# Performance work log

Measured on AMD Instinct MI355X. Metric: run time of the kernel, lower is better.

The kernel has to match this reference:

```python
import jax, jax.numpy as jnp
import numpy as np
from jax.ops import segment_sum

N_NODES = 50000


def graph_conv(src, dst, x, W, b, n_nodes):
    # DGL GraphConv with norm='both' (allow_zero_in_degree=True):
    # h = D_in^{-1/2} * A^T (D_out^{-1/2} * x) W + b, degrees clamped to >=1
    ones = jnp.ones(src.shape[0], dtype=x.dtype)
    deg_out = jnp.clip(segment_sum(ones, src, num_segments=n_nodes), 1.0)
    deg_in = jnp.clip(segment_sum(ones, dst, num_segments=n_nodes), 1.0)
    h = x * jax.lax.rsqrt(deg_out)[:, None]
    h = h @ W                      # apply weight before aggregation (mult_W first)
    m = segment_sum(h[src], dst, num_segments=n_nodes)  # sparse neighbor sum
    return m * jax.lax.rsqrt(deg_in)[:, None] + b


def setup_inputs() -> dict:
    key = jax.random.key(0)
    ks = jax.random.split(key, 10)
    n, e = N_NODES, 1600000
    d_in, h1, h2, h3 = 128, 128, 128, 64
    in_feat = jax.random.normal(ks[0], (n, d_in), dtype=jnp.float32)
    src = jax.random.randint(ks[1], (e,), 0, n, dtype=jnp.int32)
    dst = jax.random.randint(ks[2], (e,), 0, n, dtype=jnp.int32)
    s = lambda fi, fo: (1.0 / np.sqrt(fi)).astype(np.float32)
    W1 = jax.random.normal(ks[3], (d_in, h1), dtype=jnp.float32) * s(d_in, h1)
    b1 = jnp.zeros((h1,), dtype=jnp.float32)
    W2 = jax.random.normal(ks[4], (h1, h2), dtype=jnp.float32) * s(h1, h2)
    b2 = jnp.zeros((h2,), dtype=jnp.float32)
    Wf = jax.random.normal(ks[5], (h2, h3), dtype=jnp.float32) * s(h2, h3)
    bf = jnp.zeros((h3,), dtype=jnp.float32)
    return {"in_feat": in_feat, "src": src, "dst": dst,
            "W1": W1, "b1": b1, "W2": W2, "b2": b2, "Wf": Wf, "bf": bf}


def reference(in_feat, src, dst, W1, b1, W2, b2, Wf, bf):
    n = in_feat.shape[0]
    h = graph_conv(src, dst, in_feat, W1, b1, n)
    h = jax.nn.relu(h)
    # dropout(p=0.2) is identity in eval mode
    h = graph_conv(src, dst, h, W2, b2, n)
    return h @ Wf + bf
```

## Files before the change

### kernel.cpp

```cpp
#include <hip/hip_runtime.h>
#include <hip/hip_fp16.h>

#define FD 128
#define OD 64
#define KC 8
#define RN 256
#define CHUNKS 256
#define NRMAX 1024

typedef _Float16 f16x8 __attribute__((ext_vector_type(8)));
typedef float    f32x4 __attribute__((ext_vector_type(4)));


__global__ void zero_kernel(int* __restrict__ a, int n) {
    int i = blockIdx.x * 256 + threadIdx.x;
    if (i < n) a[i] = 0;
}

__global__ void rout_kernel(const int* __restrict__ cnt, float* __restrict__ r_out,
                            int N, int NW) {
    int v = blockIdx.x * 256 + threadIdx.x;
    if (v >= N) return;
    int word = v >> 1, sh = (v & 1) * 16;
    int s = 0;
    #pragma unroll
    for (int k = 0; k < KC; k++) s += (cnt[k * NW + word] >> sh) & 0xFFFF;
    r_out[v] = rsqrtf((float)max(s, 1));
}

__global__ void prescale_kernel(const float* __restrict__ X, const float* __restrict__ r_out,
                                __half* __restrict__ Xs, int n4) {
    int i = blockIdx.x * 256 + threadIdx.x;
    if (i >= n4) return;
    int v = i >> 5;
    float r = r_out[v];
    float4 t = ((const float4*)X)[i];
    __half2 h0 = __floats2half2_rn(t.x * r, t.y * r);
    __half2 h1 = __floats2half2_rn(t.z * r, t.w * r);
    ((__half2*)Xs)[2 * i]     = h0;
    ((__half2*)Xs)[2 * i + 1] = h1;
}


__global__ __launch_bounds__(1024) void region_hist_kernel(const int* __restrict__ dst,
                                                           int* __restrict__ hist_g,
                                                           int E, int NR, int CS) {
    __shared__ int hist[NRMAX];
    int c = blockIdx.x;
    for (int t = threadIdx.x; t < NR; t += 1024) hist[t] = 0;
    __syncthreads();
    int e0 = c * CS, e1 = min(e0 + CS, E);
    int nv = (e1 - e0) & ~3;
    for (int e = e0 + threadIdx.x * 4; e < e0 + nv; e += 4096) {
        int4 d = *(const int4*)(dst + e);
        atomicAdd(&hist[d.x >> 8], 1);
        atomicAdd(&hist[d.y >> 8], 1);
        atomicAdd(&hist[d.z >> 8], 1);
        atomicAdd(&hist[d.w >> 8], 1);
    }
    for (int e = e0 + nv + threadIdx.x; e < e1; e += 1024)
        atomicAdd(&hist[dst[e] >> 8], 1);
    __syncthreads();
    for (int t = threadIdx.x; t < NR; t += 1024) hist_g[c * NR + t] = hist[t];
}

__global__ __launch_bounds__(1024) void region_scan_kernel(const int* __restrict__ hist_g,
                                                           int* __restrict__ rstart,
                                                           int* __restrict__ cursor,
                                                           int NR, int E) {
    __shared__ int wsum[16];
    int tid = threadIdx.x, lane = tid & 63, w = tid >> 6;
    int total = 0;
    if (tid < NR)
        for (int c = 0; c < CHUNKS; c++) total += hist_g[c * NR + tid];
    int x = total;
    #pragma unroll
    for (int d = 1; d < 64; d <<= 1) {
        int t = __shfl_up(x, d, 64);
        if (lane >= d) x += t;
    }
    if (lane == 63) wsum[w] = x;
    __syncthreads();
    if (w == 0) {
        int s = (lane < 16) ? wsum[lane] : 0;
        #pragma unroll
        for (int d = 1; d < 16; d <<= 1) {
            int t = __shfl_up(s, d, 64);
            if (lane >= d) s += t;
        }
        if (lane < 16) wsum[lane] = s;
    }
    __syncthreads();
    int off = (w == 0) ? 0 : wsum[w - 1];
    if (tid < NR) {
        int start = x + off - total;
        rstart[tid] = start;
        int run = start;
        for (int c = 0; c < CHUNKS; c++) {
            cursor[c * NR + tid] = run;
            run += hist_g[c * NR + tid];
        }
    }
    if (tid == 0) rstart[NR] = E;
}

__global__ __launch_bounds__(1024) void partition_kernel(const int* __restrict__ src,
                                                         const int* __restrict__ dst,
                                                         const int* __restrict__ cursor,
                                                         int* __restrict__ epack,
                                                         int* __restrict__ cnt_src,
                                                         int E, int NR, int CS, int NW) {
    __shared__ int cur[NRMAX];
    int c = blockIdx.x;
    int* __restrict__ cs = cnt_src + (size_t)(blockIdx.x & (KC - 1)) * NW;
    for (int t = threadIdx.x; t < NR; t += 1024) cur[t] = cursor[c * NR + t];
    __syncthreads();
    int e0 = c * CS, e1 = min(e0 + CS, E);
    int nv = (e1 - e0) & ~3;
    for (int e = e0 + threadIdx.x * 4; e < e0 + nv; e += 4096) {
        int4 d = *(const int4*)(dst + e);
        int4 s = *(const int4*)(src + e);
        int p0 = atomicAdd(&cur[d.x >> 8], 1);
        int p1 = atomicAdd(&cur[d.y >> 8], 1);
        int p2 = atomicAdd(&cur[d.z >> 8], 1);
        int p3 = atomicAdd(&cur[d.w >> 8], 1);
        epack[p0] = ((d.x & 255) << 17) | s.x;
        epack[p1] = ((d.y & 255) << 17) | s.y;
        epack[p2] = ((d.z & 255) << 17) | s.z;
        epack[p3] = ((d.w & 255) << 17) | s.w;
        atomicAdd(&cs[s.x >> 1], 1 << ((s.x & 1) * 16));
        atomicAdd(&cs[s.y >> 1], 1 << ((s.y & 1) * 16));
        atomicAdd(&cs[s.z >> 1], 1 << ((s.z & 1) * 16));
        atomicAdd(&cs[s.w >> 1], 1 << ((s.w & 1) * 16));
    }
    for (int e = e0 + nv + threadIdx.x; e < e1; e += 1024) {
        int d = dst[e], s = src[e];
        int pos = atomicAdd(&cur[d >> 8], 1);
        epack[pos] = ((d & 255) << 17) | s;
        atomicAdd(&cs[s >> 1], 1 << ((s & 1) * 16));
    }
}

__global__ __launch_bounds__(1024) void region_sort_kernel(const int* __restrict__ epack,
                                                           const int* __restrict__ rstart,
                                                           int* __restrict__ csrc,
                                                           int* __restrict__ row_start,
                                                           float* __restrict__ r_in,
                                                           int N, int NR, int E) {
    __shared__ int cnt[RN];
    __shared__ int cur[RN];
    __shared__ int wsum[16];
    const int r = blockIdx.x, tid = threadIdx.x;
    const int lane = tid & 63, w = tid >> 6;
    const int s0 = rstart[r], s1 = rstart[r + 1];
    if (tid < RN) cnt[tid] = 0;
    __syncthreads();
    for (int e = s0 + tid; e < s1; e += 1024)
        atomicAdd(&cnt[epack[e] >> 17], 1);
    __syncthreads();
    int cv = (tid < RN) ? cnt[tid] : 0;
    int x = cv;
    #pragma unroll
    for (int d = 1; d < 64; d <<= 1) {
        int t = __shfl_up(x, d, 64);
        if (lane >= d) x += t;
    }
    if (lane == 63 && w < 4) wsum[w] = x;
    __syncthreads();
    if (tid < RN) {
        int woff = 0;
        for (int i = 0; i < w; i++) woff += wsum[i];
        int start = s0 + x - cv + woff;
        cur[tid] = start;
        int node = r * RN + tid;
        if (node < N) {
            row_start[node] = start;
            r_in[node] = rsqrtf((float)max(cv, 1));
        }
    }
    if (r == NR - 1 && tid == 0) row_start[N] = E;
    __syncthreads();
    for (int e = s0 + tid; e < s1; e += 1024) {
        int pk = epack[e];
        int pos = atomicAdd(&cur[pk >> 17], 1);
        csrc[pos] = pk & 0x1FFFF;
    }
}

__global__ __launch_bounds__(256) void agg128_kernel(const __half* __restrict__ Xs,
                                                     const float* __restrict__ r_in,
                                                     const int* __restrict__ rs,
                                                     const int* __restrict__ csrc,
                                                     __half* __restrict__ Z, int N) {
    const int lane = threadIdx.x & 63, wv = threadIdx.x >> 6;
    int v = blockIdx.x * 4 + wv;
    if (v >= N) return;
    int s0 = rs[v], s1 = rs[v + 1];
    float ax = 0.f, ay = 0.f;
    int e = s0;
    for (; e + 16 <= s1; e += 16) {
        int idx[16];
        #pragma unroll
        for (int u = 0; u < 16; u++) idx[u] = csrc[e + u];
        __half2 t[16];
        #pragma unroll
        for (int u = 0; u < 16; u++)
            t[u] = ((const __half2*)(Xs + (size_t)idx[u] * FD))[lane];
        #pragma unroll
        for (int u = 0; u < 16; u++) {
            float2 f = __half22float2(t[u]);
            ax += f.x; ay += f.y;
        }
    }
    for (; e + 4 <= s1; e += 4) {
        int idx[4];
        #pragma unroll
        for (int u = 0; u < 4; u++) idx[u] = csrc[e + u];
        __half2 t[4];
        #pragma unroll
        for (int u = 0; u < 4; u++)
            t[u] = ((const __half2*)(Xs + (size_t)idx[u] * FD))[lane];
        #pragma unroll
        for (int u = 0; u < 4; u++) {
            float2 f = __half22float2(t[u]);
            ax += f.x; ay += f.y;
        }
    }
    for (; e < s1; e++) {
        float2 f = __half22float2(((const __half2*)(Xs + (size_t)csrc[e] * FD))[lane]);
        ax += f.x; ay += f.y;
    }
    float ri = r_in[v];
    ((__half2*)(Z + (size_t)v * FD))[lane] = __floats2half2_rn(ax * ri, ay * ri);
}

__global__ __launch_bounds__(256) void agg64_kernel(const __half* __restrict__ T,
                                                    const float* __restrict__ r_in,
                                                    const int* __restrict__ rs,
                                                    const int* __restrict__ csrc,
                                                    const float* __restrict__ bc,
                                                    float* __restrict__ out, int N) {
    const int tid = threadIdx.x;
    const int lane = tid & 63, wv = tid >> 6;
    const int hf = lane >> 5, l32 = lane & 31;
    int v = blockIdx.x * 8 + wv * 2 + hf;
    if (v >= N) return;
    int s0 = rs[v], s1 = rs[v + 1];
    float ax = 0.f, ay = 0.f;
    int e = s0;
    for (; e + 8 <= s1; e += 8) {
        int idx[8];
        #pragma unroll
        for (int u = 0; u < 8; u++) idx[u] = csrc[e + u];
        __half2 t[8];
        #pragma unroll
        for (int u = 0; u < 8; u++)
            t[u] = ((const __half2*)(T + (size_t)idx[u] * OD))[l32];
        #pragma unroll
        for (int u = 0; u < 8; u++) {
            float2 f = __half22float2(t[u]);
            ax += f.x; ay += f.y;
        }
    }
    for (; e < s1; e++) {
        float2 f = __half22float2(((const __half2*)(T + (size_t)csrc[e] * OD))[l32]);
        ax += f.x; ay += f.y;
    }
    float ri = r_in[v];
    float2 o;
    o.x = ax * ri + bc[l32 * 2];
    o.y = ay * ri + bc[l32 * 2 + 1];
    ((float2*)(out + (size_t)v * OD))[l32] = o;
}

__global__ __launch_bounds__(256) void gemm1_mfma_kernel(const __half* __restrict__ Ah,
                                                         const __half* __restrict__ Bh,
                                                         const float* __restrict__ b1,
                                                         const float* __restrict__ rowscale,
                                                         __half* __restrict__ Ch,
                                                         int M, int ntiles) {
    const int w = threadIdx.x >> 6, lane = threadIdx.x & 63;
    const int l15 = lane & 15, quad = lane >> 4;
    const _Float16* B = (const _Float16*)Bh;

    f16x8 bfrag[2][4];
    #pragma unroll
    for (int nt = 0; nt < 2; nt++) {
        int col = 32 * w + 16 * nt + l15;
        #pragma unroll
        for (int kk = 0; kk < 4; kk++) {
            int kb = kk * 32 + quad * 8;
            f16x8 bf;
            #pragma unroll
            for (int j = 0; j < 8; j++) bf[j] = B[(size_t)(kb + j) * FD + col];
            bfrag[nt][kk] = bf;
        }
    }

    for (int t = blockIdx.x; t < ntiles; t += gridDim.x) {
        int row0 = t * 16;
        const _Float16* Arow = (const _Float16*)Ah + (size_t)(row0 + l15) * FD + quad * 8;
        f16x8 afrag[4];
        #pragma unroll
        for (int kk = 0; kk < 4; kk++) afrag[kk] = *(const f16x8*)(Arow + kk * 32);
        f32x4 acc0 = {0.f, 0.f, 0.f, 0.f};
        f32x4 acc1 = {0.f, 0.f, 0.f, 0.f};
        #pragma unroll
        for (int kk = 0; kk < 4; kk++) {
            acc0 = __builtin_amdgcn_mfma_f32_16x16x32_f16(afrag[kk], bfrag[0][kk], acc0, 0, 0, 0);
            acc1 = __builtin_amdgcn_mfma_f32_16x16x32_f16(afrag[kk], bfrag[1][kk], acc1, 0, 0, 0);
        }
        int c0 = 32 * w + l15, c1 = c0 + 16;
        float bb0 = b1[c0], bb1 = b1[c1];
        #pragma unroll
        for (int r = 0; r < 4; r++) {
            int row = row0 + quad * 4 + r;
            if (row < M) {
                float rsc = rowscale[row];
                Ch[(size_t)row * FD + c0] = __float2half(fmaxf(acc0[r] + bb0, 0.f) * rsc);
                Ch[(size_t)row * FD + c1] = __float2half(fmaxf(acc1[r] + bb1, 0.f) * rsc);
            }
        }
    }
}

__global__ __launch_bounds__(256) void gemm2_mfma_kernel(const __half* __restrict__ Ah,
                                                         const __half* __restrict__ Bh,
                                                         __half* __restrict__ Ch,
                                                         int M, int ntiles) {
    const int w = threadIdx.x >> 6, lane = threadIdx.x & 63;
    const int l15 = lane & 15, quad = lane >> 4;
    const _Float16* B = (const _Float16*)Bh;

    f16x8 bfrag[4];
    int col = 16 * w + l15;
    #pragma unroll
    for (int kk = 0; kk < 4; kk++) {
        int kb = kk * 32 + quad * 8;
        f16x8 bf;
        #pragma unroll
        for (int j = 0; j < 8; j++) bf[j] = B[(size_t)(kb + j) * OD + col];
        bfrag[kk] = bf;
    }

    for (int t = blockIdx.x; t < ntiles; t += gridDim.x) {
        int row0 = t * 16;
        const _Float16* Arow = (const _Float16*)Ah + (size_t)(row0 + l15) * FD + quad * 8;
        f16x8 afrag[4];
        #pragma unroll
        for (int kk = 0; kk < 4; kk++) afrag[kk] = *(const f16x8*)(Arow + kk * 32);
        f32x4 acc = {0.f, 0.f, 0.f, 0.f};
        #pragma unroll
        for (int kk = 0; kk < 4; kk++)
            acc = __builtin_amdgcn_mfma_f32_16x16x32_f16(afrag[kk], bfrag[kk], acc, 0, 0, 0);
        #pragma unroll
        for (int r = 0; r < 4; r++) {
            int row = row0 + quad * 4 + r;
            if (row < M)
                Ch[(size_t)row * OD + col] = __float2half(acc[r]);
        }
    }
}

__global__ void fold_kernel(const float* __restrict__ W2, const float* __restrict__ Wf,
                            const float* __restrict__ b2, const float* __restrict__ bf,
                            const float* __restrict__ W1,
                            __half* __restrict__ W1h, __half* __restrict__ Wch,
                            float* __restrict__ bc) {
    int idx = blockIdx.x * 256 + threadIdx.x;
    if (idx < FD * FD) W1h[idx] = __float2half(W1[idx]);
    if (idx < FD * OD) {
        int i = idx / OD, j = idx % OD;
        float s = 0.f;
        for (int k = 0; k < FD; k++) s += W2[i * FD + k] * Wf[k * OD + j];
        Wch[idx] = __float2half(s);
    }
    if (idx < OD) {
        float s = bf[idx];
        for (int k = 0; k < FD; k++) s += b2[k] * Wf[k * OD + idx];
        bc[idx] = s;
    }
}

extern "C" void kernel_launch(void* const* d_in, const int* in_sizes, int n_in,
                              void* d_out, int out_size, void* d_ws, size_t ws_size,
                              hipStream_t stream) {
    const float* in_feat = (const float*)d_in[0];
    const int*   src     = (const int*)d_in[1];
    const int*   dst     = (const int*)d_in[2];
    const float* W1      = (const float*)d_in[3];
    const float* b1      = (const float*)d_in[4];
    const float* W2      = (const float*)d_in[5];
    const float* b2      = (const float*)d_in[6];
    const float* Wf      = (const float*)d_in[7];
    const float* bf      = (const float*)d_in[8];
    float* out = (float*)d_out;

    const int N = in_sizes[0] / FD;
    const int E = in_sizes[1];
    const int NR = (N + RN - 1) / RN;
    const int NW = (N + 1) / 2;
    const int CS = (((E + CHUNKS - 1) / CHUNKS) + 3) & ~3;

    char* ws = (char*)d_ws;
    size_t off = 0;
    auto alloc = [&](size_t bytes) -> void* {
        void* p = ws + off;
        off += (bytes + 255) / 256 * 256;
        return p;
    };
    int*    cnt_src = (int*)alloc((size_t)KC * NW * 4);
    int*    epack   = (int*)alloc((size_t)E * 4);
    __half* tbuf    = (__half*)cnt_src;
    float*  r_out   = (float*)alloc((size_t)N * 4);
    float*  r_in    = (float*)alloc((size_t)N * 4);
    int*    hist_g  = (int*)alloc((size_t)CHUNKS * NR * 4);
    int*    cursor  = (int*)alloc((size_t)CHUNKS * NR * 4);
    int*    rstart  = (int*)alloc((size_t)(NR + 1) * 4);
    int*    csrc    = (int*)alloc((size_t)E * 4);
    int*    row_start = (int*)alloc((size_t)(N + 1) * 4);
    __half* z1h     = (__half*)alloc((size_t)N * FD * 2);
    __half* y1h     = (__half*)alloc((size_t)N * FD * 2);
    __half* Xs      = (__half*)alloc((size_t)N * FD * 2);
    __half* W1h     = (__half*)alloc((size_t)FD * FD * 2);
    __half* Wch     = (__half*)alloc((size_t)FD * OD * 2);
    float*  bc      = (float*)alloc((size_t)OD * 4);
    (void)ws_size; (void)n_in; (void)out_size;

    const int gN = (N + 255) / 256;
    const int ntiles = (N + 15) / 16;
    const int gemmgrid = ntiles < 1024 ? ntiles : 1024;

    zero_kernel<<<(KC * NW + 255) / 256, 256, 0, stream>>>(cnt_src, KC * NW);
    region_hist_kernel<<<CHUNKS, 1024, 0, stream>>>(dst, hist_g, E, NR, CS);
    region_scan_kernel<<<1, 1024, 0, stream>>>(hist_g, rstart, cursor, NR, E);
    partition_kernel<<<CHUNKS, 1024, 0, stream>>>(src, dst, cursor, epack, cnt_src, E, NR, CS, NW);
    region_sort_kernel<<<NR, 1024, 0, stream>>>(epack, rstart, csrc, row_start, r_in, N, NR, E);
    rout_kernel<<<gN, 256, 0, stream>>>(cnt_src, r_out, N, NW);

    fold_kernel<<<(FD * FD + 255) / 256, 256, 0, stream>>>(W2, Wf, b2, bf, W1, W1h, Wch, bc);

    prescale_kernel<<<(N * 32 + 255) / 256, 256, 0, stream>>>(in_feat, r_out, Xs, N * 32);
    agg128_kernel<<<(N + 3) / 4, 256, 0, stream>>>(Xs, r_in, row_start, csrc, z1h, N);

    gemm1_mfma_kernel<<<gemmgrid, 256, 0, stream>>>(z1h, W1h, b1, r_out, y1h, N, ntiles);
    gemm2_mfma_kernel<<<gemmgrid, 256, 0, stream>>>(y1h, Wch, tbuf, N, ntiles);

    agg64_kernel<<<(N + 7) / 8, 256, 0, stream>>>(tbuf, r_in, row_start, csrc, bc, out, N);
}
```

Before: 305.8 us.

## Compute out-degrees via region bucketing of src instead of global atomics

Out-degree counting no longer uses global atomics into packed 16-bit counters spread over replicated arrays. Source IDs are now histogrammed by region alongside dst, scanned, and partitioned into a byte-packed buffer. A per-region kernel then counts them in shared memory. This removes the zero kernel and the scattered global atomics, but adds more shared atomics in hist and partition, an extra scan pass, and byte scatter writes.

```diff
diff --git a/kernel.cpp b/kernel.cpp
--- a/kernel.cpp
+++ b/kernel.cpp
@@ -3,7 +3,6 @@
 
 #define FD 128
 #define OD 64
-#define KC 8
 #define RN 256
 #define CHUNKS 256
 #define NRMAX 1024
@@ -11,22 +10,6 @@
 typedef _Float16 f16x8 __attribute__((ext_vector_type(8)));
 typedef float    f32x4 __attribute__((ext_vector_type(4)));
 
-
-__global__ void zero_kernel(int* __restrict__ a, int n) {
-    int i = blockIdx.x * 256 + threadIdx.x;
-    if (i < n) a[i] = 0;
-}
-
-__global__ void rout_kernel(const int* __restrict__ cnt, float* __restrict__ r_out,
-                            int N, int NW) {
-    int v = blockIdx.x * 256 + threadIdx.x;
-    if (v >= N) return;
-    int word = v >> 1, sh = (v & 1) * 16;
-    int s = 0;
-    #pragma unroll
-    for (int k = 0; k < KC; k++) s += (cnt[k * NW + word] >> sh) & 0xFFFF;
-    r_out[v] = rsqrtf((float)max(s, 1));
-}
 
 __global__ void prescale_kernel(const float* __restrict__ X, const float* __restrict__ r_out,
                                 __half* __restrict__ Xs, int n4) {
@@ -42,31 +25,47 @@
 }
 
 
-__global__ __launch_bounds__(1024) void region_hist_kernel(const int* __restrict__ dst,
+__global__ __launch_bounds__(1024) void region_hist_kernel(const int* __restrict__ src,
+                                                           const int* __restrict__ dst,
                                                            int* __restrict__ hist_g,
+                                                           int* __restrict__ hist_gs,
                                                            int E, int NR, int CS) {
     __shared__ int hist[NRMAX];
+    __shared__ int hist_s[NRMAX];
     int c = blockIdx.x;
-    for (int t = threadIdx.x; t < NR; t += 1024) hist[t] = 0;
+    for (int t = threadIdx.x; t < NR; t += 1024) { hist[t] = 0; hist_s[t] = 0; }
     __syncthreads();
     int e0 = c * CS, e1 = min(e0 + CS, E);
     int nv = (e1 - e0) & ~3;
     for (int e = e0 + threadIdx.x * 4; e < e0 + nv; e += 4096) {
         int4 d = *(const int4*)(dst + e);
+        int4 s = *(const int4*)(src + e);
         atomicAdd(&hist[d.x >> 8], 1);
         atomicAdd(&hist[d.y >> 8], 1);
         atomicAdd(&hist[d.z >> 8], 1);
         atomicAdd(&hist[d.w >> 8], 1);
-    }
-    for (int e = e0 + nv + threadIdx.x; e < e1; e += 1024)
+        atomicAdd(&hist_s[s.x >> 8], 1);
+        atomicAdd(&hist_s[s.y >> 8], 1);
+        atomicAdd(&hist_s[s.z >> 8], 1);
+        atomicAdd(&hist_s[s.w >> 8], 1);
+    }
+    for (int e = e0 + nv + threadIdx.x; e < e1; e += 1024) {
         atomicAdd(&hist[dst[e] >> 8], 1);
-    __syncthreads();
-    for (int t = threadIdx.x; t < NR; t += 1024) hist_g[c * NR + t] = hist[t];
+        atomicAdd(&hist_s[src[e] >> 8], 1);
+    }
+    __syncthreads();
+    for (int t = threadIdx.x; t < NR; t += 1024) {
+        hist_g[c * NR + t]  = hist[t];
+        hist_gs[c * NR + t] = hist_s[t];
+    }
 }
 
 __global__ __launch_bounds__(1024) void region_scan_kernel(const int* __restrict__ hist_g,
+                                                           const int* __restrict__ hist_gs,
                                                            int* __restrict__ rstart,
                                                            int* __restrict__ cursor,
+                                                           int* __restrict__ sstart,
+                                                           int* __restrict__ scursor,
                                                            int NR, int E) {
     __shared__ int wsum[16];
     int tid = threadIdx.x, lane = tid & 63, w = tid >> 6;
@@ -102,18 +101,55 @@
         }
     }
     if (tid == 0) rstart[NR] = E;
+    __syncthreads();
+    total = 0;
+    if (tid < NR)
+        for (int c = 0; c < CHUNKS; c++) total += hist_gs[c * NR + tid];
+    x = total;
+    #pragma unroll
+    for (int d = 1; d < 64; d <<= 1) {
+        int t = __shfl_up(x, d, 64);
+        if (lane >= d) x += t;
+    }
+    if (lane == 63) wsum[w] = x;
+    __syncthreads();
+    if (w == 0) {
+        int s = (lane < 16) ? wsum[lane] : 0;
+        #pragma unroll
+        for (int d = 1; d < 16; d <<= 1) {
+            int t = __shfl_up(s, d, 64);
+            if (lane >= d) s += t;
+        }
+        if (lane < 16) wsum[lane] = s;
+    }
+    __syncthreads();
+    off = (w == 0) ? 0 : wsum[w - 1];
+    if (tid < NR) {
+        int start = x + off - total;
+        sstart[tid] = start;
+        int run = start;
+        for (int c = 0; c < CHUNKS; c++) {
+            scursor[c * NR + tid] = run;
+            run += hist_gs[c * NR + tid];
+        }
+    }
+    if (tid == 0) sstart[NR] = E;
 }
 
 __global__ __launch_bounds__(1024) void partition_kernel(const int* __restrict__ src,
                                                          const int* __restrict__ dst,
                                                          const int* __restrict__ cursor,
+                                                         const int* __restrict__ scursor,
                                                          int* __restrict__ epack,
-                                                         int* __restrict__ cnt_src,
-                                                         int E, int NR, int CS, int NW) {
+                                                         unsigned char* __restrict__ spack,
+                                                         int E, int NR, int CS) {
     __shared__ int cur[NRMAX];
+    __shared__ int scur[NRMAX];
     int c = blockIdx.x;
-    int* __restrict__ cs = cnt_src + (size_t)(blockIdx.x & (KC - 1)) * NW;
-    for (int t = threadIdx.x; t < NR; t += 1024) cur[t] = cursor[c * NR + t];
+    for (int t = threadIdx.x; t < NR; t += 1024) {
+        cur[t]  = cursor[c * NR + t];
+        scur[t] = scursor[c * NR + t];
+    }
     __syncthreads();
     int e0 = c * CS, e1 = min(e0 + CS, E);
     int nv = (e1 - e0) & ~3;
@@ -128,16 +164,21 @@
         epack[p1] = ((d.y & 255) << 17) | s.y;
         epack[p2] = ((d.z & 255) << 17) | s.z;
         epack[p3] = ((d.w & 255) << 17) | s.w;
-        atomicAdd(&cs[s.x >> 1], 1 << ((s.x & 1) * 16));
-        atomicAdd(&cs[s.y >> 1], 1 << ((s.y & 1) * 16));
-        atomicAdd(&cs[s.z >> 1], 1 << ((s.z & 1) * 16));
-        atomicAdd(&cs[s.w >> 1], 1 << ((s.w & 1) * 16));
+        int q0 = atomicAdd(&scur[s.x >> 8], 1);
+        int q1 = atomicAdd(&scur[s.y >> 8], 1);
+        int q2 = atomicAdd(&scur[s.z >> 8], 1);
+        int q3 = atomicAdd(&scur[s.w >> 8], 1);
+        spack[q0] = (unsigned char)(s.x & 255);
+        spack[q1] = (unsigned char)(s.y & 255);
+        spack[q2] = (unsigned char)(s.z & 255);
+        spack[q3] = (unsigned char)(s.w & 255);
     }
     for (int e = e0 + nv + threadIdx.x; e < e1; e += 1024) {
         int d = dst[e], s = src[e];
         int pos = atomicAdd(&cur[d >> 8], 1);
         epack[pos] = ((d & 255) << 17) | s;
-        atomicAdd(&cs[s >> 1], 1 << ((s & 1) * 16));
+        int qos = atomicAdd(&scur[s >> 8], 1);
+        spack[qos] = (unsigned char)(s & 255);
     }
 }
 
@@ -185,6 +226,21 @@
         int pos = atomicAdd(&cur[pk >> 17], 1);
         csrc[pos] = pk & 0x1FFFF;
     }
+}
+
+__global__ __launch_bounds__(256) void rout2_kernel(const unsigned char* __restrict__ spack,
+                                                    const int* __restrict__ sstart,
+                                                    float* __restrict__ r_out, int N) {
+    __shared__ int cnt[RN];
+    const int r = blockIdx.x, tid = threadIdx.x;
+    const int s0 = sstart[r], s1 = sstart[r + 1];
+    cnt[tid] = 0;
+    __syncthreads();
+    for (int e = s0 + tid; e < s1; e += 256)
+        atomicAdd(&cnt[spack[e]], 1);
+    __syncthreads();
+    int node = r * RN + tid;
+    if (node < N) r_out[node] = rsqrtf((float)max(cnt[tid], 1));
 }
 
 __global__ __launch_bounds__(256) void agg128_kernel(const __half* __restrict__ Xs,
@@ -399,7 +455,6 @@
     const int N = in_sizes[0] / FD;
     const int E = in_sizes[1];
     const int NR = (N + RN - 1) / RN;
-    const int NW = (N + 1) / 2;
     const int CS = (((E + CHUNKS - 1) / CHUNKS) + 3) & ~3;
 
     char* ws = (char*)d_ws;
@@ -409,14 +464,17 @@
         off += (bytes + 255) / 256 * 256;
         return p;
     };
-    int*    cnt_src = (int*)alloc((size_t)KC * NW * 4);
+    unsigned char* spack = (unsigned char*)alloc((size_t)E);
     int*    epack   = (int*)alloc((size_t)E * 4);
-    __half* tbuf    = (__half*)cnt_src;
+    __half* tbuf    = (__half*)spack;
     float*  r_out   = (float*)alloc((size_t)N * 4);
     float*  r_in    = (float*)alloc((size_t)N * 4);
     int*    hist_g  = (int*)alloc((size_t)CHUNKS * NR * 4);
+    int*    hist_gs = (int*)alloc((size_t)CHUNKS * NR * 4);
     int*    cursor  = (int*)alloc((size_t)CHUNKS * NR * 4);
+    int*    scursor = (int*)alloc((size_t)CHUNKS * NR * 4);
     int*    rstart  = (int*)alloc((size_t)(NR + 1) * 4);
+    int*    sstart  = (int*)alloc((size_t)(NR + 1) * 4);
     int*    csrc    = (int*)alloc((size_t)E * 4);
     int*    row_start = (int*)alloc((size_t)(N + 1) * 4);
     __half* z1h     = (__half*)alloc((size_t)N * FD * 2);
@@ -427,16 +485,14 @@
     float*  bc      = (float*)alloc((size_t)OD * 4);
     (void)ws_size; (void)n_in; (void)out_size;
 
-    const int gN = (N + 255) / 256;
     const int ntiles = (N + 15) / 16;
     const int gemmgrid = ntiles < 1024 ? ntiles : 1024;
 
-    zero_kernel<<<(KC * NW + 255) / 256, 256, 0, stream>>>(cnt_src, KC * NW);
-    region_hist_kernel<<<CHUNKS, 1024, 0, stream>>>(dst, hist_g, E, NR, CS);
-    region_scan_kernel<<<1, 1024, 0, stream>>>(hist_g, rstart, cursor, NR, E);
-    partition_kernel<<<CHUNKS, 1024, 0, stream>>>(src, dst, cursor, epack, cnt_src, E, NR, CS, NW);
+    region_hist_kernel<<<CHUNKS, 1024, 0, stream>>>(src, dst, hist_g, hist_gs, E, NR, CS);
+    region_scan_kernel<<<1, 1024, 0, stream>>>(hist_g, hist_gs, rstart, cursor, sstart, scursor, NR, E);
+    partition_kernel<<<CHUNKS, 1024, 0, stream>>>(src, dst, cursor, scursor, epack, spack, E, NR, CS);
     region_sort_kernel<<<NR, 1024, 0, stream>>>(epack, rstart, csrc, row_start, r_in, N, NR, E);
-    rout_kernel<<<gN, 256, 0, stream>>>(cnt_src, r_out, N, NW);
+    rout2_kernel<<<NR, 256, 0, stream>>>(spack, sstart, r_out, N);
 
     fold_kernel<<<(FD * FD + 255) / 256, 256, 0, stream>>>(W2, Wf, b2, bf, W1, W1h, Wch, bc);
 
```

Measured after the change: 282.0 us. 7.8% less time.
